# Kernel optimization log

Measured on AMD Instinct MI355X. Metric: run time of the kernel, lower is better.

## Reference

```python
import jax, jax.numpy as jnp
import numpy as np

BETA = 5.5
ALPHA = 0.5

def _l2norm(x, eps=1e-12):
    # matches torch F.normalize(dim=-1): x / max(||x||, eps)
    n = jnp.sqrt(jnp.sum(x * x, axis=-1, keepdims=True))
    return x / jnp.maximum(n, eps)

def setup_inputs() -> dict:
    key = jax.random.key(0)
    k1, k2 = jax.random.split(key)
    query_features = jax.random.normal(k1, (4096, 512), dtype=jnp.float32)
    support_keys = jax.random.normal(k2, (16384, 512), dtype=jnp.float32)
    return {"query_features": query_features, "support_keys": support_keys}

def reference(query_features, support_keys):
    cache_keys = _l2norm(support_keys)              # (N, D)
    q = _l2norm(query_features)                     # (B, D)
    affinity = jnp.einsum('bd,nd->bn', q, cache_keys)   # (B, N) cosine sims
    affinity = jnp.exp(-BETA * (1.0 - affinity))
    retrieved = jnp.einsum('bn,nd->bd', affinity, cache_keys)  # (B, D)
    return query_features + ALPHA * retrieved
```

## Files before the change

kernel.cpp:

```cpp
#include <hip/hip_runtime.h>
#include <cstdint>
#include <cstddef>

#define BETA 5.5f
#define ALPHA 0.5f

constexpr int D   = 512;
constexpr int NB  = 4096;
constexpr int NK  = 16384;
constexpr int BQ  = 64;
constexpr int BN  = 64;
constexpr int NSPLIT = 4;
constexpr int NRANGE = NK / NSPLIT;
constexpr int CHUNKS = NRANGE / BN;
constexpr int KROW = D + 8;
constexpr int PROW = BN + 8;

typedef __attribute__((ext_vector_type(8)))  short    short8;
typedef __attribute__((ext_vector_type(4)))  float    floatx4;
typedef __attribute__((ext_vector_type(4)))  uint32_t uint4v;
typedef __attribute__((ext_vector_type(2)))  uint32_t uint2v;

__device__ inline uint32_t f2bf1(float f) {
  union { float f; uint32_t u; } v; v.f = f;
  return (v.u + 0x7FFFu + ((v.u >> 16) & 1u)) >> 16;
}
__device__ inline uint32_t pack2(float a, float b) {
  return f2bf1(a) | (f2bf1(b) << 16);
}

__device__ inline void load_lds16(const void* g, void* l) {
  __builtin_amdgcn_global_load_lds(
      (const __attribute__((address_space(1))) uint32_t*)g,
      (__attribute__((address_space(3))) uint32_t*)l, 16, 0, 0);
}

__global__ void norm_q_kernel(const float* __restrict__ q,
                              float* __restrict__ out,
                              unsigned short* __restrict__ Qn) {
  const int wave = threadIdx.x >> 6, lane = threadIdx.x & 63;
  const int row = blockIdx.x * 4 + wave;
  const float4* qr = (const float4*)(q + (size_t)row * D);
  float4 a = qr[lane * 2];
  float4 b = qr[lane * 2 + 1];
  float ss = a.x*a.x + a.y*a.y + a.z*a.z + a.w*a.w
           + b.x*b.x + b.y*b.y + b.z*b.z + b.w*b.w;
#pragma unroll
  for (int m = 32; m >= 1; m >>= 1) ss += __shfl_xor(ss, m, 64);
  const float sc = 1.0f / fmaxf(sqrtf(ss), 1e-12f);
  float4* orow = (float4*)(out + (size_t)row * D);
  orow[lane * 2]     = a;
  orow[lane * 2 + 1] = b;
  uint4v w;
  w.x = pack2(a.x*sc, a.y*sc); w.y = pack2(a.z*sc, a.w*sc);
  w.z = pack2(b.x*sc, b.y*sc); w.w = pack2(b.z*sc, b.w*sc);
  *(uint4v*)(Qn + (size_t)row * D + lane * 8) = w;
}

__global__ void norm_k_kernel(const float* __restrict__ k,
                              unsigned short* __restrict__ Kn,
                              unsigned short* __restrict__ KnT) {
  __shared__ unsigned short tile[64 * KROW];
  const int wave = threadIdx.x >> 6, lane = threadIdx.x & 63;
  const int n0 = blockIdx.x * 64;
#pragma unroll
  for (int i = 0; i < 4; ++i) {
    const int rl = wave * 4 + i;
    const int n  = n0 + rl;
    const float4* kr = (const float4*)(k + (size_t)n * D);
    float4 a = kr[lane * 2], b = kr[lane * 2 + 1];
    float ss = a.x*a.x + a.y*a.y + a.z*a.z + a.w*a.w
             + b.x*b.x + b.y*b.y + b.z*b.z + b.w*b.w;
#pragma unroll
    for (int m = 32; m >= 1; m >>= 1) ss += __shfl_xor(ss, m, 64);
    const float sc = 1.0f / fmaxf(sqrtf(ss), 1e-12f);
    uint4v w;
    w.x = pack2(a.x*sc, a.y*sc); w.y = pack2(a.z*sc, a.w*sc);
    w.z = pack2(b.x*sc, b.y*sc); w.w = pack2(b.z*sc, b.w*sc);
    *(uint4v*)(Kn + (size_t)n * D + lane * 8) = w;
    *(uint4v*)&tile[rl * KROW + lane * 8]     = w;
  }
  __syncthreads();
  const int dsub = threadIdx.x >> 3;
  const int nl   = (threadIdx.x & 7) * 8;
#pragma unroll
  for (int iter = 0; iter < 4; ++iter) {
    const int d = iter * 128 + ((dsub + nl) & 127);
    uint4v w;
    w.x = (uint32_t)tile[(nl+0)*KROW + d] | ((uint32_t)tile[(nl+1)*KROW + d] << 16);
    w.y = (uint32_t)tile[(nl+2)*KROW + d] | ((uint32_t)tile[(nl+3)*KROW + d] << 16);
    w.z = (uint32_t)tile[(nl+4)*KROW + d] | ((uint32_t)tile[(nl+5)*KROW + d] << 16);
    w.w = (uint32_t)tile[(nl+6)*KROW + d] | ((uint32_t)tile[(nl+7)*KROW + d] << 16);
    *(uint4v*)(KnT + (size_t)d * NK + n0 + nl) = w;
  }
}

__global__ __launch_bounds__(512, 2) void fused_kernel(
    const unsigned short* __restrict__ Qn,
    const unsigned short* __restrict__ Kn,
    const unsigned short* __restrict__ KnT,
    float* __restrict__ out) {
  __shared__ unsigned short K_lds[2][BN * KROW];
  __shared__ unsigned short P_lds[2][BQ * PROW];

  const int tid  = threadIdx.x;
  const int wave = tid >> 6, lane = tid & 63;
  const int l15  = lane & 15, quad = lane >> 4;
  const int nsplit = blockIdx.x & (NSPLIT - 1);
  const int qtile  = blockIdx.x >> 2;
  const int q0     = qtile * BQ;
  const int nbase  = nsplit * NRANGE;

  if (wave < 4) {
    const int sw = wave;
    const int qh = wave & 1, nh = wave >> 1;
    short8 qf[2][16];
    {
      const unsigned short* qrow0 = Qn + (size_t)(q0 + qh * 32 + l15) * D + quad * 8;
#pragma unroll
      for (int qt = 0; qt < 2; ++qt)
#pragma unroll
        for (int kb = 0; kb < 16; ++kb)
          qf[qt][kb] = *(const short8*)(qrow0 + (size_t)qt * 16 * D + kb * 32);
    }

    floatx4 sacc[2][2];

    auto stage = [&](int ch, int buf) {
#pragma unroll
      for (int i = 0; i < 16; ++i) {
        const int row = sw * 16 + i;
        load_lds16(Kn + (size_t)(nbase + ch * BN + row) * D + lane * 8,
                   &K_lds[buf][row * KROW]);
      }
    };
    auto a_read8 = [&](int buf, int kb0, short8* af) {
#pragma unroll
      for (int i = 0; i < 4; ++i) {
        af[2*i]   = *(const short8*)&K_lds[buf][(nh*32 +      l15) * KROW + (kb0+i)*32 + quad*8];
        af[2*i+1] = *(const short8*)&K_lds[buf][(nh*32 + 16 + l15) * KROW + (kb0+i)*32 + quad*8];
      }
    };
    auto g1c = [&](const short8* af, int kb0) {
#pragma unroll
      for (int i = 0; i < 4; ++i) {
        sacc[0][0] = __builtin_amdgcn_mfma_f32_16x16x32_bf16(af[2*i],   qf[0][kb0+i], sacc[0][0], 0, 0, 0);
        sacc[0][1] = __builtin_amdgcn_mfma_f32_16x16x32_bf16(af[2*i],   qf[1][kb0+i], sacc[0][1], 0, 0, 0);
        sacc[1][0] = __builtin_amdgcn_mfma_f32_16x16x32_bf16(af[2*i+1], qf[0][kb0+i], sacc[1][0], 0, 0, 0);
        sacc[1][1] = __builtin_amdgcn_mfma_f32_16x16x32_bf16(af[2*i+1], qf[1][kb0+i], sacc[1][1], 0, 0, 0);
      }
    };
    auto gemm1_region_st = [&](int buf, int sch, int sbuf, bool do_stage) {
#pragma unroll
      for (int nt = 0; nt < 2; ++nt)
#pragma unroll
        for (int qt = 0; qt < 2; ++qt) sacc[nt][qt] = (floatx4){0.f, 0.f, 0.f, 0.f};
      short8 afA[8], afB[8];
      a_read8(buf, 0, afA);
      a_read8(buf, 4, afB);
      if (do_stage) stage(sch, sbuf);
      g1c(afA, 0);
      a_read8(buf, 8, afA);
      g1c(afB, 4);
      a_read8(buf, 12, afB);
      g1c(afA, 8);
      g1c(afB, 12);
    };
    auto exp_pw = [&](int slot) {
#pragma unroll
      for (int qt = 0; qt < 2; ++qt)
#pragma unroll
        for (int nt = 0; nt < 2; ++nt) {
          const floatx4 s = sacc[nt][qt];
          uint2v w;
          w.x = pack2(__expf(BETA * (s[0] - 1.f)), __expf(BETA * (s[1] - 1.f)));
          w.y = pack2(__expf(BETA * (s[2] - 1.f)), __expf(BETA * (s[3] - 1.f)));
          *(uint2v*)&P_lds[slot][(qh*32 + qt*16 + l15) * PROW + nh*32 + nt*16 + quad*4] = w;
        }
    };

    __builtin_amdgcn_s_setprio(1);

    stage(0, 0);
    asm volatile("s_waitcnt vmcnt(0)" ::: "memory");
    asm volatile("s_barrier" ::: "memory");
    gemm1_region_st(0, 1, 1, true);
    exp_pw(0);
    asm volatile("s_waitcnt vmcnt(0) lgkmcnt(0)" ::: "memory");
    asm volatile("s_barrier" ::: "memory");

#pragma unroll 1
    for (int r = 0; r + 2 < CHUNKS; ++r) {
      gemm1_region_st((r + 1) & 1, r + 2, r & 1, true);
      exp_pw((r + 1) & 1);
      asm volatile("s_waitcnt vmcnt(0) lgkmcnt(0)" ::: "memory");
      asm volatile("s_barrier" ::: "memory");
    }
    gemm1_region_st((CHUNKS - 1) & 1, 0, 0, false);
    exp_pw((CHUNKS - 1) & 1);
    asm volatile("s_waitcnt lgkmcnt(0)" ::: "memory");
    asm volatile("s_barrier" ::: "memory");
    __builtin_amdgcn_s_setprio(0);
  } else {
    const int w4 = wave - 4;
    floatx4 oacc[4][8] = {};
    short8 ktf[2][8];
    const unsigned short* ktb = KnT + (size_t)(w4 * 128 + l15) * NK + nbase + quad * 8;

    auto ldKT = [&](short8* kt, int c, int kb2) {
#pragma unroll
      for (int td = 0; td < 8; ++td)
        kt[td] = *(const short8*)(ktb + (size_t)td * 16 * NK + c * BN + kb2 * 32);
    };
    auto pf_read = [&](int slot, int kb2, short8* pf) {
#pragma unroll
      for (int tr = 0; tr < 4; ++tr)
        pf[tr] = *(const short8*)&P_lds[slot][(tr*16 + l15) * PROW + kb2*32 + quad*8];
    };
    auto g2c = [&](const short8* pf, const short8* kt) {
#pragma unroll
      for (int td = 0; td < 8; ++td)
#pragma unroll
        for (int tr = 0; tr < 4; ++tr)
          oacc[tr][td] = __builtin_amdgcn_mfma_f32_16x16x32_bf16(
              pf[tr], kt[td], oacc[tr][td], 0, 0, 0);
    };

    ldKT(ktf[0], 0, 0); ldKT(ktf[1], 0, 1);
    asm volatile("s_barrier" ::: "memory");
    asm volatile("s_barrier" ::: "memory");

#pragma unroll 1
    for (int r = 0; r + 2 < CHUNKS; ++r) {
      short8 pf0[4], pf1[4];
      pf_read(r & 1, 0, pf0);
      pf_read(r & 1, 1, pf1);
      g2c(pf0, ktf[0]);
      ldKT(ktf[0], r + 1, 0);
      g2c(pf1, ktf[1]);
      ldKT(ktf[1], r + 1, 1);
      asm volatile("s_barrier" ::: "memory");
    }
    {
      const int r = CHUNKS - 2;
      short8 pf0[4], pf1[4];
      pf_read(r & 1, 0, pf0);
      pf_read(r & 1, 1, pf1);
      g2c(pf0, ktf[0]);
      ldKT(ktf[0], CHUNKS - 1, 0);
      g2c(pf1, ktf[1]);
      ldKT(ktf[1], CHUNKS - 1, 1);
      asm volatile("s_barrier" ::: "memory");
    }
    {
      short8 pf0[4], pf1[4];
      pf_read((CHUNKS - 1) & 1, 0, pf0);
      pf_read((CHUNKS - 1) & 1, 1, pf1);
      g2c(pf0, ktf[0]);
      g2c(pf1, ktf[1]);
    }

    const int colbase = w4 * 128 + l15;
#pragma unroll
    for (int tr = 0; tr < 4; ++tr)
#pragma unroll
      for (int td = 0; td < 8; ++td)
#pragma unroll
        for (int r4 = 0; r4 < 4; ++r4)
          atomicAdd(out + (size_t)(q0 + tr*16 + quad*4 + r4) * D + colbase + td*16,
                    ALPHA * oacc[tr][td][r4]);
  }
}

extern "C" void kernel_launch(void* const* d_in, const int* in_sizes, int n_in,
                              void* d_out, int out_size, void* d_ws, size_t ws_size,
                              hipStream_t stream) {
  (void)in_sizes; (void)n_in; (void)out_size; (void)ws_size;
  const float* q = (const float*)d_in[0];
  const float* k = (const float*)d_in[1];
  float* out = (float*)d_out;
  unsigned short* Qn  = (unsigned short*)d_ws;
  unsigned short* Kn  = Qn + (size_t)NB * D;
  unsigned short* KnT = Kn + (size_t)NK * D;

  hipLaunchKernelGGL(norm_q_kernel, dim3(NB / 4),  dim3(256),  0, stream, q, out, Qn);
  hipLaunchKernelGGL(norm_k_kernel, dim3(NK / 64), dim3(1024), 0, stream, k, Kn, KnT);
  hipLaunchKernelGGL(fused_kernel, dim3((NB / BQ) * NSPLIT), dim3(512), 0, stream,
                     Qn, Kn, KnT, out);
}
```

Measured before the change: 265.8 us.

## Give each GEMM1 wave a full 64-query by 16-key tile and relax occupancy

```diff
diff --git a/kernel.cpp b/kernel.cpp
--- a/kernel.cpp
+++ b/kernel.cpp
@@ -95,7 +95,7 @@
   }
 }
 
-__global__ __launch_bounds__(512, 2) void fused_kernel(
+__global__ __launch_bounds__(512, 1) void fused_kernel(
     const unsigned short* __restrict__ Qn,
     const unsigned short* __restrict__ Kn,
     const unsigned short* __restrict__ KnT,
@@ -113,18 +113,17 @@
 
   if (wave < 4) {
     const int sw = wave;
-    const int qh = wave & 1, nh = wave >> 1;
-    short8 qf[2][16];
+    short8 qf[4][16];
     {
-      const unsigned short* qrow0 = Qn + (size_t)(q0 + qh * 32 + l15) * D + quad * 8;
-#pragma unroll
-      for (int qt = 0; qt < 2; ++qt)
+      const unsigned short* qrow0 = Qn + (size_t)(q0 + l15) * D + quad * 8;
+#pragma unroll
+      for (int qt = 0; qt < 4; ++qt)
 #pragma unroll
         for (int kb = 0; kb < 16; ++kb)
           qf[qt][kb] = *(const short8*)(qrow0 + (size_t)qt * 16 * D + kb * 32);
     }
 
-    floatx4 sacc[2][2];
+    floatx4 sacc[4];
 
     auto stage = [&](int ch, int buf) {
 #pragma unroll
@@ -134,49 +133,33 @@
                    &K_lds[buf][row * KROW]);
       }
     };
-    auto a_read8 = [&](int buf, int kb0, short8* af) {
-#pragma unroll
-      for (int i = 0; i < 4; ++i) {
-        af[2*i]   = *(const short8*)&K_lds[buf][(nh*32 +      l15) * KROW + (kb0+i)*32 + quad*8];
-        af[2*i+1] = *(const short8*)&K_lds[buf][(nh*32 + 16 + l15) * KROW + (kb0+i)*32 + quad*8];
+    auto a_read = [&](int buf, int kb) -> short8 {
+      return *(const short8*)&K_lds[buf][(sw*16 + l15) * KROW + kb*32 + quad*8];
+    };
+    auto gemm1_region_st = [&](int buf, int sch, int sbuf, bool do_stage) {
+#pragma unroll
+      for (int qt = 0; qt < 4; ++qt) sacc[qt] = (floatx4){0.f, 0.f, 0.f, 0.f};
+      short8 af[16];
+#pragma unroll
+      for (int kb = 0; kb < 16; ++kb) af[kb] = a_read(buf, kb);
+      if (do_stage) stage(sch, sbuf);
+#pragma unroll
+      for (int kb = 0; kb < 16; ++kb) {
+        sacc[0] = __builtin_amdgcn_mfma_f32_16x16x32_bf16(af[kb], qf[0][kb], sacc[0], 0, 0, 0);
+        sacc[1] = __builtin_amdgcn_mfma_f32_16x16x32_bf16(af[kb], qf[1][kb], sacc[1], 0, 0, 0);
+        sacc[2] = __builtin_amdgcn_mfma_f32_16x16x32_bf16(af[kb], qf[2][kb], sacc[2], 0, 0, 0);
+        sacc[3] = __builtin_amdgcn_mfma_f32_16x16x32_bf16(af[kb], qf[3][kb], sacc[3], 0, 0, 0);
       }
     };
-    auto g1c = [&](const short8* af, int kb0) {
-#pragma unroll
-      for (int i = 0; i < 4; ++i) {
-        sacc[0][0] = __builtin_amdgcn_mfma_f32_16x16x32_bf16(af[2*i],   qf[0][kb0+i], sacc[0][0], 0, 0, 0);
-        sacc[0][1] = __builtin_amdgcn_mfma_f32_16x16x32_bf16(af[2*i],   qf[1][kb0+i], sacc[0][1], 0, 0, 0);
-        sacc[1][0] = __builtin_amdgcn_mfma_f32_16x16x32_bf16(af[2*i+1], qf[0][kb0+i], sacc[1][0], 0, 0, 0);
-        sacc[1][1] = __builtin_amdgcn_mfma_f32_16x16x32_bf16(af[2*i+1], qf[1][kb0+i], sacc[1][1], 0, 0, 0);
+    auto exp_pw = [&](int slot) {
+#pragma unroll
+      for (int qt = 0; qt < 4; ++qt) {
+        const floatx4 s = sacc[qt];
+        uint2v w;
+        w.x = pack2(__expf(BETA * (s[0] - 1.f)), __expf(BETA * (s[1] - 1.f)));
+        w.y = pack2(__expf(BETA * (s[2] - 1.f)), __expf(BETA * (s[3] - 1.f)));
+        *(uint2v*)&P_lds[slot][(qt*16 + l15) * PROW + sw*16 + quad*4] = w;
       }
-    };
-    auto gemm1_region_st = [&](int buf, int sch, int sbuf, bool do_stage) {
-#pragma unroll
-      for (int nt = 0; nt < 2; ++nt)
-#pragma unroll
-        for (int qt = 0; qt < 2; ++qt) sacc[nt][qt] = (floatx4){0.f, 0.f, 0.f, 0.f};
-      short8 afA[8], afB[8];
-      a_read8(buf, 0, afA);
-      a_read8(buf, 4, afB);
-      if (do_stage) stage(sch, sbuf);
-      g1c(afA, 0);
-      a_read8(buf, 8, afA);
-      g1c(afB, 4);
-      a_read8(buf, 12, afB);
-      g1c(afA, 8);
-      g1c(afB, 12);
-    };
-    auto exp_pw = [&](int slot) {
-#pragma unroll
-      for (int qt = 0; qt < 2; ++qt)
-#pragma unroll
-        for (int nt = 0; nt < 2; ++nt) {
-          const floatx4 s = sacc[nt][qt];
-          uint2v w;
-          w.x = pack2(__expf(BETA * (s[0] - 1.f)), __expf(BETA * (s[1] - 1.f)));
-          w.y = pack2(__expf(BETA * (s[2] - 1.f)), __expf(BETA * (s[3] - 1.f)));
-          *(uint2v*)&P_lds[slot][(qh*32 + qt*16 + l15) * PROW + nh*32 + nt*16 + quad*4] = w;
-        }
     };
 
     __builtin_amdgcn_s_setprio(1);
```

New measurement: 391.6 us. 1.47x slower.
